# Kernel tuning notes

Measured on AMD Instinct MI355X. Metric: run time of the kernel, lower is better.

Reference implementation:

```python
import jax, jax.numpy as jnp
import numpy as np

V, D, H, L, MAXS = 32000, 768, 12, 6, 2048
HD = D // H  # 64
FF = 4 * D
B, S = 8, 1024
EPS = 1e-5


def _make_pe():
    pos = np.arange(MAXS, dtype=np.float32)[:, None]
    div = np.exp(np.arange(0, D, 2, dtype=np.float32) * (-np.log(10000.0) / D))
    pe = np.zeros((MAXS, D), dtype=np.float32)
    pe[:, 0::2] = np.sin(pos * div)
    pe[:, 1::2] = np.cos(pos * div)
    return jnp.asarray(pe)


def setup_inputs() -> dict:
    key = jax.random.key(0)
    ks = jax.random.split(key, 16)
    sc = 0.02
    return {
        "tokens": jax.random.randint(ks[0], (B, S), 0, V),
        "k_mask": jnp.ones((B, S), dtype=jnp.int32),
        "emb": jax.random.normal(ks[1], (V, D), jnp.float32) * sc,
        "pe": _make_pe(),
        "ln1_s": jnp.ones((L, D), jnp.float32),
        "ln1_b": jnp.zeros((L, D), jnp.float32),
        "wq": jax.random.normal(ks[2], (L, H, D, HD), jnp.float32) * sc,
        "wk": jax.random.normal(ks[3], (L, H, D, HD), jnp.float32) * sc,
        "wv": jax.random.normal(ks[4], (L, H, D, HD), jnp.float32) * sc,
        "wo": jax.random.normal(ks[5], (L, D, D), jnp.float32) * sc,
        "ln2_s": jnp.ones((L, D), jnp.float32),
        "ln2_b": jnp.zeros((L, D), jnp.float32),
        "w1": jax.random.normal(ks[6], (L, D, FF), jnp.float32) * sc,
        "b1": jnp.zeros((L, FF), jnp.float32),
        "w2": jax.random.normal(ks[7], (L, FF, D), jnp.float32) * sc,
        "b2": jnp.zeros((L, D), jnp.float32),
    }


def _ln(x, s, b):
    m = jnp.mean(x, axis=-1, keepdims=True)
    v = jnp.var(x, axis=-1, keepdims=True)
    return (x - m) * jax.lax.rsqrt(v + EPS) * s + b


def _forward(tokens, k_mask, emb, pe, ln1_s, ln1_b, wq, wk, wv, wo,
             ln2_s, ln2_b, w1, b1, w2, b2):
    x = emb[tokens] + pe[None, :tokens.shape[1], :]  # [B,S,D]
    mask = (k_mask != 0)[:, None, None, :]  # [B,1,1,S]
    for l in range(L):
        xn = _ln(x, ln1_s[l], ln1_b[l])
        q = jnp.einsum('bsd,hde->bhse', xn, wq[l])
        k = jnp.einsum('bsd,hde->bhse', xn, wk[l])
        v = jnp.einsum('bsd,hde->bhse', xn, wv[l])
        scores = jnp.einsum('bhse,bhte->bhst', q, k) / (HD ** 0.5)
        scores = jnp.where(mask, scores, -jnp.inf)
        attn = jax.nn.softmax(scores, axis=-1)
        o = jnp.einsum('bhst,bhte->bhse', attn, v)  # [B,H,S,HD]
        o = o.transpose(0, 2, 1, 3).reshape(x.shape)  # concat heads -> [B,S,D]
        x = x + o @ wo[l]
        xn = _ln(x, ln2_s[l], ln2_b[l])
        h = jax.nn.gelu(xn @ w1[l] + b1[l], approximate=False)
        x = x + h @ w2[l] + b2[l]
    return x


def reference(tokens, k_mask, emb, pe, ln1_s, ln1_b, wq, wk, wv, wo,
              ln2_s, ln2_b, w1, b1, w2, b2):
    return _forward(tokens, k_mask, emb, pe, ln1_s, ln1_b, wq, wk, wv, wo,
                    ln2_s, ln2_b, w1, b1, w2, b2)
```

## Files before the change

kernel.cpp:

```cpp
#include <hip/hip_runtime.h>
#include <math.h>

typedef unsigned short u16;
typedef unsigned int u32;
typedef __attribute__((ext_vector_type(8))) __bf16 bf16x8;
typedef __attribute__((ext_vector_type(4))) float f32x4;
typedef __attribute__((ext_vector_type(8))) unsigned short ushort8v;
typedef __attribute__((ext_vector_type(4))) float float4v;
typedef __attribute__((ext_vector_type(4))) unsigned short u16x4;

typedef const __attribute__((address_space(1))) void gvoid_t;
typedef __attribute__((address_space(3))) void lvoid_t;

#define MFMA(a, b, c) __builtin_amdgcn_mfma_f32_16x16x32_bf16((a), (b), (c), 0, 0, 0)

__device__ __forceinline__ u16 f2bf(float f) {
  __bf16 h = (__bf16)f;
  return __builtin_bit_cast(u16, h);
}

__device__ __forceinline__ void stage64(const u16* g, int ldg, u16* lds, int rows, int tid) {
  int w = tid >> 6, l = tid & 63;
  int lr = l >> 3;
  int cb = (l & 7) << 4;
  for (int it = 0; it < rows; it += 32) {
    int rbase = it + w * 8;
    int r = rbase + lr;
    int scb = cb ^ ((r & 7) << 4);
    const char* gp = (const char*)(g + (size_t)r * ldg) + scb;
    char* lp = (char*)lds + (size_t)rbase * 128;
    __builtin_amdgcn_global_load_lds((gvoid_t*)gp, (lvoid_t*)lp, 16, 0, 0);
  }
}

__device__ __forceinline__ bf16x8 ldsfrag(const u16* base, int row, int e0) {
  int boff = row * 128 + (((e0) << 1) ^ ((row & 7) << 4));
  return *(const bf16x8*)((const char*)base + boff);
}

__global__ void embed_kernel(const int* __restrict__ tok, const float* __restrict__ emb,
                             const float* __restrict__ pe, float* __restrict__ xf) {
  int row = blockIdx.x;
  int tid = threadIdx.x;
  int t = tok[row];
  int spos = row & 1023;
  float4v e = ((const float4v*)(emb + (size_t)t * 768))[tid];
  float4v p = ((const float4v*)(pe + (size_t)spos * 768))[tid];
  float4v r;
  r.x = e.x + p.x; r.y = e.y + p.y; r.z = e.z + p.z; r.w = e.w + p.w;
  ((float4v*)(xf + (size_t)row * 768))[tid] = r;
}

__global__ void ln_kernel(const float* __restrict__ x, const float* __restrict__ sc,
                          const float* __restrict__ bi, u16* __restrict__ out) {
  int row = blockIdx.x;
  int tid = threadIdx.x;
  float4v v = ((const float4v*)(x + (size_t)row * 768))[tid];
  float s = v.x + v.y + v.z + v.w;
  float s2 = v.x * v.x + v.y * v.y + v.z * v.z + v.w * v.w;
  #pragma unroll
  for (int off = 32; off >= 1; off >>= 1) {
    s += __shfl_down(s, off);
    s2 += __shfl_down(s2, off);
  }
  __shared__ float red[8];
  if ((tid & 63) == 0) { red[tid >> 6] = s; red[4 + (tid >> 6)] = s2; }
  __syncthreads();
  float S = red[0] + red[1] + red[2];
  float S2 = red[4] + red[5] + red[6];
  float m = S * (1.0f / 768.0f);
  float var = S2 * (1.0f / 768.0f) - m * m;
  float rs = rsqrtf(var + 1e-5f);
  float4v sv = ((const float4v*)sc)[tid];
  float4v bv = ((const float4v*)bi)[tid];
  u16x4 ov;
  ov.x = f2bf((v.x - m) * rs * sv.x + bv.x);
  ov.y = f2bf((v.y - m) * rs * sv.y + bv.y);
  ov.z = f2bf((v.z - m) * rs * sv.z + bv.z);
  ov.w = f2bf((v.w - m) * rs * sv.w + bv.w);
  *(u16x4*)(out + (size_t)row * 768 + tid * 4) = ov;
}

__global__ void convT_kernel(const float* __restrict__ src, u16* __restrict__ dst,
                             int N, int K, long long sz, long long dz) {
  src += (size_t)blockIdx.z * sz;
  dst += (size_t)blockIdx.z * dz;
  __shared__ float t[32][33];
  int n0 = blockIdx.x * 32, k0 = blockIdx.y * 32;
  int tid = threadIdx.x;
  int tx = tid & 31, ty = tid >> 5;
  for (int r = ty; r < 32; r += 8) t[r][tx] = src[(size_t)(k0 + r) * N + n0 + tx];
  __syncthreads();
  for (int r = ty; r < 32; r += 8) dst[(size_t)(n0 + r) * K + k0 + tx] = f2bf(t[tx][r]);
}

__global__ void convqkvT_kernel(const float* __restrict__ wq, const float* __restrict__ wk,
                                const float* __restrict__ wv, u16* __restrict__ dst,
                                long long wz, long long dz) {
  __shared__ float t[32][33];
  int n0 = blockIdx.x * 32, k0 = blockIdx.y * 32;
  int which = n0 / 768;
  int r0 = n0 % 768;
  int h = r0 >> 6, e0 = r0 & 63;
  const float* src = which == 0 ? wq : (which == 1 ? wk : wv);
  src += (size_t)blockIdx.z * wz;
  dst += (size_t)blockIdx.z * dz;
  int tid = threadIdx.x;
  int tx = tid & 31, ty = tid >> 5;
  for (int r = ty; r < 32; r += 8) t[r][tx] = src[(size_t)(h * 768 + k0 + r) * 64 + e0 + tx];
  __syncthreads();
  for (int r = ty; r < 32; r += 8) dst[(size_t)(n0 + r) * 768 + k0 + tx] = f2bf(t[tx][r]);
}

__global__ void transpose_v_kernel(const u16* __restrict__ v, u16* __restrict__ vt) {
  __shared__ u16 t[64][72];
  int bh = blockIdx.x, sc = blockIdx.y;
  int tid = threadIdx.x;
  const u16* src = v + ((size_t)bh * 1024 + sc * 64) * 64;
  int sl = tid >> 2, e0 = (tid & 3) * 16;
  ushort8v a = *(const ushort8v*)(src + (size_t)sl * 64 + e0);
  ushort8v b = *(const ushort8v*)(src + (size_t)sl * 64 + e0 + 8);
  #pragma unroll
  for (int j = 0; j < 8; ++j) t[sl][e0 + j] = a[j];
  #pragma unroll
  for (int j = 0; j < 8; ++j) t[sl][e0 + 8 + j] = b[j];
  __syncthreads();
  int e = tid >> 2, s0 = (tid & 3) * 16;
  ushort8v o0, o1;
  #pragma unroll
  for (int j = 0; j < 8; ++j) o0[j] = t[s0 + j][e];
  #pragma unroll
  for (int j = 0; j < 8; ++j) o1[j] = t[s0 + 8 + j][e];
  u16* dst = vt + ((size_t)bh * 64 + e) * 1024 + sc * 64 + s0;
  *(ushort8v*)dst = o0;
  *(ushort8v*)(dst + 8) = o1;
}

template <int MODE, int NK>
__global__ __launch_bounds__(256) void gemm128(
    const u16* __restrict__ A, int lda, const u16* __restrict__ Wt, int ldb, int kOuter,
    float* __restrict__ xf, u16* __restrict__ outb, const float* __restrict__ bias,
    u16* __restrict__ qb, u16* __restrict__ kb, u16* __restrict__ vb) {
  __shared__ alignas(16) u16 As[128 * 64];
  __shared__ alignas(16) u16 Bs[128 * 64];
  int tid = threadIdx.x, lane = tid & 63, w = tid >> 6;
  int wm = w >> 1, wn = w & 1;
  int m0 = blockIdx.x * 128, n0 = blockIdx.y * 128;
  f32x4 acc[4][4] = {};
  int lr = lane >> 3;
  int cb = (lane & 7) << 4;
  int sws = cb ^ (lr << 4);
  const char* pA = (const char*)(A + (size_t)m0 * lda) + (size_t)(w * 8 + lr) * (lda * 2) + sws;
  const char* pB = (const char*)(Wt + (size_t)n0 * ldb) + (size_t)(w * 8 + lr) * (ldb * 2) + sws;
  char* dA = (char*)As + w * 1024;
  char* dB = (char*)Bs + w * 1024;
  int arow = wm * 64 + (lane & 15);
  int brow = wn * 64 + (lane & 15);
  int e0 = (lane >> 4) * 8;
  for (int c = 0; c < kOuter; ++c) {
    #pragma unroll
    for (int kt = 0; kt < NK; ++kt) {
      __syncthreads();
      #pragma unroll
      for (int i = 0; i < 4; ++i) {
        __builtin_amdgcn_global_load_lds((gvoid_t*)(pA + (size_t)i * 32 * (lda * 2)),
                                         (lvoid_t*)(dA + i * 4096), 16, 0, 0);
        __builtin_amdgcn_global_load_lds((gvoid_t*)(pB + (size_t)i * 32 * (ldb * 2)),
                                         (lvoid_t*)(dB + i * 4096), 16, 0, 0);
      }
      pA += 128; pB += 128;
      __syncthreads();
      #pragma unroll
      for (int kk = 0; kk < 2; ++kk) {
        bf16x8 af[4], bfr[4];
        #pragma unroll
        for (int mt = 0; mt < 4; ++mt) af[mt] = ldsfrag(As, arow + mt * 16, kk * 32 + e0);
        #pragma unroll
        for (int nt = 0; nt < 4; ++nt) bfr[nt] = ldsfrag(Bs, brow + nt * 16, kk * 32 + e0);
        #pragma unroll
        for (int mt = 0; mt < 4; ++mt)
          #pragma unroll
          for (int nt = 0; nt < 4; ++nt)
            acc[mt][nt] = MFMA(af[mt], bfr[nt], acc[mt][nt]);
      }
    }
  }
  int rbase = m0 + wm * 64 + ((lane >> 4) << 2);
  int cbase = n0 + wn * 64 + (lane & 15);
  if constexpr (MODE == 0) {
    int which = n0 / 768;
    u16* dstb = which == 0 ? qb : (which == 1 ? kb : vb);
    int cloc = cbase - which * 768;
    #pragma unroll
    for (int mt = 0; mt < 4; ++mt) {
      #pragma unroll
      for (int nt = 0; nt < 4; ++nt) {
        int rr = cloc + nt * 16;
        int h = rr >> 6, e = rr & 63;
        #pragma unroll
        for (int reg = 0; reg < 4; ++reg) {
          int row = rbase + mt * 16 + reg;
          int b = row >> 10, s = row & 1023;
          dstb[((size_t)(b * 12 + h) * 1024 + s) * 64 + e] = f2bf(acc[mt][nt][reg]);
        }
      }
    }
  } else if constexpr (MODE == 2) {
    #pragma unroll
    for (int mt = 0; mt < 4; ++mt) {
      #pragma unroll
      for (int nt = 0; nt < 4; ++nt) {
        int col = cbase + nt * 16;
        float bb = bias[col];
        #pragma unroll
        for (int reg = 0; reg < 4; ++reg) {
          int row = rbase + mt * 16 + reg;
          float t = acc[mt][nt][reg] + bb;
          float u = t * fmaf(t * t, 0.044715f, 1.0f);
          float ex = __builtin_amdgcn_exp2f(u * -2.3022156f);
          float g = t * __builtin_amdgcn_rcpf(1.0f + ex);
          outb[(size_t)row * 3072 + col] = f2bf(g);
        }
      }
    }
  } else {
    #pragma unroll
    for (int mt = 0; mt < 4; ++mt) {
      #pragma unroll
      for (int nt = 0; nt < 4; ++nt) {
        int col = cbase + nt * 16;
        float bb = (MODE == 3) ? bias[col] : 0.0f;
        #pragma unroll
        for (int reg = 0; reg < 4; ++reg) {
          int row = rbase + mt * 16 + reg;
          xf[(size_t)row * 768 + col] += acc[mt][nt][reg] + bb;
        }
      }
    }
  }
}

__global__ __launch_bounds__(256) void flash64(
    const u16* __restrict__ q, const u16* __restrict__ k, const u16* __restrict__ vt,
    const int* __restrict__ kmask, u16* __restrict__ o) {
  __shared__ alignas(16) u16 Qs[64 * 64];
  __shared__ alignas(16) u16 Ks[2][64 * 64];
  __shared__ alignas(16) u16 Vs[2][64 * 64];
  __shared__ alignas(16) u16 Ps[64 * 64];
  int tid = threadIdx.x, lane = tid & 63, w = tid >> 6;
  int lc = lane & 15;
  int bh = blockIdx.x, q0 = blockIdx.y * 64;
  int b = bh / 12, h = bh % 12;

  stage64(q + ((size_t)bh * 1024 + q0) * 64, 64, Qs, 64, tid);
  __syncthreads();
  int qrow = w * 16 + lc;
  int e0 = (lane >> 4) * 8;
  bf16x8 aq0 = ldsfrag(Qs, qrow, e0);
  bf16x8 aq1 = ldsfrag(Qs, qrow, 32 + e0);

  bf16x8 ones;
  #pragma unroll
  for (int j = 0; j < 8; ++j) ones[j] = (__bf16)1.0f;

  f32x4 oacc[4] = {};
  f32x4 lacc = {};
  const float SCL = 0.125f * 1.44269504f;
  const float SH = -3.0f * 1.44269504f;
  int prow_base = w * 16 + ((lane >> 4) << 2);

  stage64(k + (size_t)bh * 1024 * 64, 64, Ks[0], 64, tid);
  stage64(vt + (size_t)bh * 64 * 1024, 1024, Vs[0], 64, tid);

  for (int kt = 0; kt < 16; ++kt) {
    asm volatile("s_waitcnt vmcnt(0)" ::: "memory");
    __builtin_amdgcn_sched_barrier(0);
    __builtin_amdgcn_s_barrier();
    __builtin_amdgcn_sched_barrier(0);
    const u16* Kc = Ks[kt & 1];
    const u16* Vc = Vs[kt & 1];

    f32x4 sacc[4] = {};
    #pragma unroll
    for (int nt = 0; nt < 4; ++nt) {
      bf16x8 bk = ldsfrag(Kc, nt * 16 + lc, e0);
      sacc[nt] = MFMA(aq0, bk, sacc[nt]);
    }
    #pragma unroll
    for (int nt = 0; nt < 4; ++nt) {
      bf16x8 bk = ldsfrag(Kc, nt * 16 + lc, 32 + e0);
      sacc[nt] = MFMA(aq1, bk, sacc[nt]);
    }

    if (kt + 1 < 16) {
      stage64(k + ((size_t)bh * 1024 + (kt + 1) * 64) * 64, 64, Ks[(kt + 1) & 1], 64, tid);
      stage64(vt + (size_t)bh * 64 * 1024 + (kt + 1) * 64, 1024, Vs[(kt + 1) & 1], 64, tid);
    }

    #pragma unroll
    for (int nt = 0; nt < 4; ++nt) {
      int c = nt * 16 + lc;
      float mk = kmask[b * 1024 + kt * 64 + c] ? SH : -1e30f;
      #pragma unroll
      for (int r = 0; r < 4; ++r) {
        float p = __builtin_amdgcn_exp2f(fmaf(sacc[nt][r], SCL, mk));
        int prow = prow_base + r;
        int boff = prow * 128 + ((c << 1) ^ ((prow & 7) << 4));
        *(u16*)((char*)Ps + boff) = f2bf(p);
      }
    }

    bf16x8 ap0 = ldsfrag(Ps, qrow, e0);
    bf16x8 ap1 = ldsfrag(Ps, qrow, 32 + e0);
    lacc = MFMA(ap0, ones, lacc);
    lacc = MFMA(ap1, ones, lacc);
    #pragma unroll
    for (int et = 0; et < 4; ++et) {
      bf16x8 bv = ldsfrag(Vc, et * 16 + lc, e0);
      oacc[et] = MFMA(ap0, bv, oacc[et]);
    }
    #pragma unroll
    for (int et = 0; et < 4; ++et) {
      bf16x8 bv = ldsfrag(Vc, et * 16 + lc, 32 + e0);
      oacc[et] = MFMA(ap1, bv, oacc[et]);
    }
  }

  float rl[4];
  #pragma unroll
  for (int r = 0; r < 4; ++r) rl[r] = __builtin_amdgcn_rcpf(lacc[r]);
  int orow_base = q0 + prow_base;
  #pragma unroll
  for (int et = 0; et < 4; ++et) {
    int e = et * 16 + lc;
    #pragma unroll
    for (int r = 0; r < 4; ++r) {
      int row = orow_base + r;
      o[((size_t)(b * 1024 + row)) * 768 + h * 64 + e] = f2bf(oacc[et][r] * rl[r]);
    }
  }
}

__global__ void copy_kernel(const float* __restrict__ src, float* __restrict__ dst) {
  size_t i = (size_t)blockIdx.x * blockDim.x + threadIdx.x;
  ((float4v*)dst)[i] = ((const float4v*)src)[i];
}

extern "C" void kernel_launch(void* const* d_in, const int* in_sizes, int n_in,
                              void* d_out, int out_size, void* d_ws, size_t ws_size,
                              hipStream_t stream) {
  const int* tokens = (const int*)d_in[0];
  const int* kmask = (const int*)d_in[1];
  const float* emb = (const float*)d_in[2];
  const float* pe = (const float*)d_in[3];
  const float* ln1_s = (const float*)d_in[4];
  const float* ln1_b = (const float*)d_in[5];
  const float* wq = (const float*)d_in[6];
  const float* wk = (const float*)d_in[7];
  const float* wv = (const float*)d_in[8];
  const float* wo = (const float*)d_in[9];
  const float* ln2_s = (const float*)d_in[10];
  const float* ln2_b = (const float*)d_in[11];
  const float* w1 = (const float*)d_in[12];
  const float* b1 = (const float*)d_in[13];
  const float* w2 = (const float*)d_in[14];
  const float* b2 = (const float*)d_in[15];

  char* ws = (char*)d_ws;
  float* xf = (float*)ws;
  u16* xn   = (u16*)(ws + 25165824);
  u16* qb   = (u16*)(ws + 37748736);
  u16* kb   = (u16*)(ws + 50331648);
  u16* vb   = (u16*)(ws + 62914560);
  u16* vtb  = (u16*)(ws + 75497472);
  u16* ob   = (u16*)(ws + 88080384);
  u16* ffh  = (u16*)(ws + 100663296);

  const size_t SZ_QKV = (size_t)2304 * 768;
  const size_t SZ_O   = (size_t)768 * 768;
  const size_t SZ_F1  = (size_t)3072 * 768;
  const size_t SZ_F2  = (size_t)768 * 3072;
  const size_t NEED = 150994944 + 2 * 6 * (SZ_QKV + SZ_O + SZ_F1 + SZ_F2);
  bool pre = ws_size >= NEED;
  int nz = pre ? 6 : 1;
  u16* wqkvt = (u16*)(ws + 150994944);
  u16* wot   = wqkvt + (size_t)nz * SZ_QKV;
  u16* w1t   = wot + (size_t)nz * SZ_O;
  u16* w2t   = w1t + (size_t)nz * SZ_F1;

  embed_kernel<<<8192, 192, 0, stream>>>(tokens, emb, pe, xf);

  if (pre) {
    convqkvT_kernel<<<dim3(72, 24, 6), 256, 0, stream>>>(wq, wk, wv, wqkvt, 589824LL, (long long)SZ_QKV);
    convT_kernel<<<dim3(24, 24, 6), 256, 0, stream>>>(wo, wot, 768, 768, 589824LL, (long long)SZ_O);
    convT_kernel<<<dim3(96, 24, 6), 256, 0, stream>>>(w1, w1t, 3072, 768, 2359296LL, (long long)SZ_F1);
    convT_kernel<<<dim3(24, 96, 6), 256, 0, stream>>>(w2, w2t, 768, 3072, 2359296LL, (long long)SZ_F2);
  }

  for (int l = 0; l < 6; ++l) {
    size_t woff_qkv = (size_t)l * 12 * 768 * 64;
    size_t woff_o = (size_t)l * 768 * 768;
    size_t woff_ff = (size_t)l * 768 * 3072;
    const u16* wt_qkv_l = wqkvt + (pre ? (size_t)l * SZ_QKV : 0);
    const u16* wt_o_l   = wot   + (pre ? (size_t)l * SZ_O   : 0);
    const u16* wt_1_l   = w1t   + (pre ? (size_t)l * SZ_F1  : 0);
    const u16* wt_2_l   = w2t   + (pre ? (size_t)l * SZ_F2  : 0);

    if (!pre) {
      convqkvT_kernel<<<dim3(72, 24, 1), 256, 0, stream>>>(wq + woff_qkv, wk + woff_qkv, wv + woff_qkv, (u16*)wt_qkv_l, 0LL, 0LL);
      convT_kernel<<<dim3(24, 24, 1), 256, 0, stream>>>(wo + woff_o, (u16*)wt_o_l, 768, 768, 0LL, 0LL);
      convT_kernel<<<dim3(96, 24, 1), 256, 0, stream>>>(w1 + woff_ff, (u16*)wt_1_l, 3072, 768, 0LL, 0LL);
      convT_kernel<<<dim3(24, 96, 1), 256, 0, stream>>>(w2 + woff_ff, (u16*)wt_2_l, 768, 3072, 0LL, 0LL);
    }

    ln_kernel<<<8192, 192, 0, stream>>>(xf, ln1_s + l * 768, ln1_b + l * 768, xn);
    gemm128<0, 6><<<dim3(64, 18, 1), 256, 0, stream>>>(xn, 768, wt_qkv_l, 768, 2, nullptr, nullptr, nullptr, qb, kb, vb);
    transpose_v_kernel<<<dim3(96, 16), 256, 0, stream>>>(vb, vtb);
    flash64<<<dim3(96, 16), 256, 0, stream>>>(qb, kb, vtb, kmask, ob);
    gemm128<1, 6><<<dim3(64, 6, 1), 256, 0, stream>>>(ob, 768, wt_o_l, 768, 2, xf, nullptr, nullptr, nullptr, nullptr, nullptr);
    ln_kernel<<<8192, 192, 0, stream>>>(xf, ln2_s + l * 768, ln2_b + l * 768, xn);
    gemm128<2, 6><<<dim3(64, 24, 1), 256, 0, stream>>>(xn, 768, wt_1_l, 768, 2, nullptr, ffh, b1 + l * 3072, nullptr, nullptr, nullptr);
    gemm128<3, 6><<<dim3(64, 6, 1), 256, 0, stream>>>(ffh, 3072, wt_2_l, 3072, 8, xf, nullptr, b2 + l * 768, nullptr, nullptr, nullptr);
  }

  copy_kernel<<<6144, 256, 0, stream>>>(xf, (float*)d_out);
}
```

Baseline: 1.594 ms.

## Use 128-query flash tiles, 64-wide N tiles for D-output GEMMs, fuse final copy

Flash attention now processes 128 query rows per block (two 64-row halves per wave), so each staged K/V tile is reused twice and the K/V loads per query are halved. The Q tile is staged through the Ps and Ks buffers to save LDS. The output-projection and FFN2 GEMMs use 64-wide N tiles, doubling their block count (384 to 768) to fill more CUs. The final copy kernel is removed by having the last FFN2 epilogue also write its result to the output buffer. The trade-offs are fewer attention blocks (768), more register pressure from the doubled accumulators, and lower per-block MFMA density in the narrow GEMMs.

```diff
diff --git a/kernel.cpp b/kernel.cpp
--- a/kernel.cpp
+++ b/kernel.cpp
@@ -136,17 +136,20 @@
   *(ushort8v*)(dst + 8) = o1;
 }
 
-template <int MODE, int NK>
+template <int MODE, int NK, int BN>
 __global__ __launch_bounds__(256) void gemm128(
     const u16* __restrict__ A, int lda, const u16* __restrict__ Wt, int ldb, int kOuter,
     float* __restrict__ xf, u16* __restrict__ outb, const float* __restrict__ bias,
-    u16* __restrict__ qb, u16* __restrict__ kb, u16* __restrict__ vb) {
+    u16* __restrict__ qb, u16* __restrict__ kb, u16* __restrict__ vb,
+    float* __restrict__ outf) {
+  constexpr int NT = BN / 32;
+  constexpr int NBAND = BN / 2;
   __shared__ alignas(16) u16 As[128 * 64];
-  __shared__ alignas(16) u16 Bs[128 * 64];
+  __shared__ alignas(16) u16 Bs[BN * 64];
   int tid = threadIdx.x, lane = tid & 63, w = tid >> 6;
   int wm = w >> 1, wn = w & 1;
-  int m0 = blockIdx.x * 128, n0 = blockIdx.y * 128;
-  f32x4 acc[4][4] = {};
+  int m0 = blockIdx.x * 128, n0 = blockIdx.y * BN;
+  f32x4 acc[4][NT] = {};
   int lr = lane >> 3;
   int cb = (lane & 7) << 4;
   int sws = cb ^ (lr << 4);
@@ -155,38 +158,39 @@
   char* dA = (char*)As + w * 1024;
   char* dB = (char*)Bs + w * 1024;
   int arow = wm * 64 + (lane & 15);
-  int brow = wn * 64 + (lane & 15);
+  int brow = wn * NBAND + (lane & 15);
   int e0 = (lane >> 4) * 8;
   for (int c = 0; c < kOuter; ++c) {
     #pragma unroll
     for (int kt = 0; kt < NK; ++kt) {
       __syncthreads();
       #pragma unroll
-      for (int i = 0; i < 4; ++i) {
+      for (int i = 0; i < 4; ++i)
         __builtin_amdgcn_global_load_lds((gvoid_t*)(pA + (size_t)i * 32 * (lda * 2)),
                                          (lvoid_t*)(dA + i * 4096), 16, 0, 0);
+      #pragma unroll
+      for (int i = 0; i < BN / 32; ++i)
         __builtin_amdgcn_global_load_lds((gvoid_t*)(pB + (size_t)i * 32 * (ldb * 2)),
                                          (lvoid_t*)(dB + i * 4096), 16, 0, 0);
-      }
       pA += 128; pB += 128;
       __syncthreads();
       #pragma unroll
       for (int kk = 0; kk < 2; ++kk) {
-        bf16x8 af[4], bfr[4];
+        bf16x8 af[4], bfr[NT];
         #pragma unroll
         for (int mt = 0; mt < 4; ++mt) af[mt] = ldsfrag(As, arow + mt * 16, kk * 32 + e0);
         #pragma unroll
-        for (int nt = 0; nt < 4; ++nt) bfr[nt] = ldsfrag(Bs, brow + nt * 16, kk * 32 + e0);
+        for (int nt = 0; nt < NT; ++nt) bfr[nt] = ldsfrag(Bs, brow + nt * 16, kk * 32 + e0);
         #pragma unroll
         for (int mt = 0; mt < 4; ++mt)
           #pragma unroll
-          for (int nt = 0; nt < 4; ++nt)
+          for (int nt = 0; nt < NT; ++nt)
             acc[mt][nt] = MFMA(af[mt], bfr[nt], acc[mt][nt]);
       }
     }
   }
   int rbase = m0 + wm * 64 + ((lane >> 4) << 2);
-  int cbase = n0 + wn * 64 + (lane & 15);
+  int cbase = n0 + wn * NBAND + (lane & 15);
   if constexpr (MODE == 0) {
     int which = n0 / 768;
     u16* dstb = which == 0 ? qb : (which == 1 ? kb : vb);
@@ -194,7 +198,7 @@
     #pragma unroll
     for (int mt = 0; mt < 4; ++mt) {
       #pragma unroll
-      for (int nt = 0; nt < 4; ++nt) {
+      for (int nt = 0; nt < NT; ++nt) {
         int rr = cloc + nt * 16;
         int h = rr >> 6, e = rr & 63;
         #pragma unroll
@@ -209,7 +213,7 @@
     #pragma unroll
     for (int mt = 0; mt < 4; ++mt) {
       #pragma unroll
-      for (int nt = 0; nt < 4; ++nt) {
+      for (int nt = 0; nt < NT; ++nt) {
         int col = cbase + nt * 16;
         float bb = bias[col];
         #pragma unroll
@@ -227,44 +231,51 @@
     #pragma unroll
     for (int mt = 0; mt < 4; ++mt) {
       #pragma unroll
-      for (int nt = 0; nt < 4; ++nt) {
+      for (int nt = 0; nt < NT; ++nt) {
         int col = cbase + nt * 16;
         float bb = (MODE == 3) ? bias[col] : 0.0f;
         #pragma unroll
         for (int reg = 0; reg < 4; ++reg) {
           int row = rbase + mt * 16 + reg;
-          xf[(size_t)row * 768 + col] += acc[mt][nt][reg] + bb;
+          size_t idx = (size_t)row * 768 + col;
+          float nv = xf[idx] + acc[mt][nt][reg] + bb;
+          xf[idx] = nv;
+          if (MODE == 3 && outf) outf[idx] = nv;
         }
       }
     }
   }
 }
 
-__global__ __launch_bounds__(256) void flash64(
+__global__ __launch_bounds__(256) void flash128(
     const u16* __restrict__ q, const u16* __restrict__ k, const u16* __restrict__ vt,
     const int* __restrict__ kmask, u16* __restrict__ o) {
-  __shared__ alignas(16) u16 Qs[64 * 64];
   __shared__ alignas(16) u16 Ks[2][64 * 64];
   __shared__ alignas(16) u16 Vs[2][64 * 64];
   __shared__ alignas(16) u16 Ps[64 * 64];
   int tid = threadIdx.x, lane = tid & 63, w = tid >> 6;
   int lc = lane & 15;
-  int bh = blockIdx.x, q0 = blockIdx.y * 64;
-  int b = bh / 12, h = bh % 12;
-
-  stage64(q + ((size_t)bh * 1024 + q0) * 64, 64, Qs, 64, tid);
+  int bh = blockIdx.x, q0 = blockIdx.y * 128;
+  int b = bh / 12, hd = bh % 12;
+
+  stage64(q + ((size_t)bh * 1024 + q0) * 64, 64, Ps, 64, tid);
+  stage64(q + ((size_t)bh * 1024 + q0 + 64) * 64, 64, Ks[0], 64, tid);
   __syncthreads();
   int qrow = w * 16 + lc;
   int e0 = (lane >> 4) * 8;
-  bf16x8 aq0 = ldsfrag(Qs, qrow, e0);
-  bf16x8 aq1 = ldsfrag(Qs, qrow, 32 + e0);
+  bf16x8 aq[2][2];
+  aq[0][0] = ldsfrag(Ps, qrow, e0);
+  aq[0][1] = ldsfrag(Ps, qrow, 32 + e0);
+  aq[1][0] = ldsfrag(Ks[0], qrow, e0);
+  aq[1][1] = ldsfrag(Ks[0], qrow, 32 + e0);
+  __syncthreads();
 
   bf16x8 ones;
   #pragma unroll
   for (int j = 0; j < 8; ++j) ones[j] = (__bf16)1.0f;
 
-  f32x4 oacc[4] = {};
-  f32x4 lacc = {};
+  f32x4 oacc[2][4] = {};
+  f32x4 lacc[2] = {};
   const float SCL = 0.125f * 1.44269504f;
   const float SH = -3.0f * 1.44269504f;
   int prow_base = w * 16 + ((lane >> 4) << 2);
@@ -280,16 +291,15 @@
     const u16* Kc = Ks[kt & 1];
     const u16* Vc = Vs[kt & 1];
 
-    f32x4 sacc[4] = {};
+    f32x4 sacc[2][4] = {};
     #pragma unroll
     for (int nt = 0; nt < 4; ++nt) {
-      bf16x8 bk = ldsfrag(Kc, nt * 16 + lc, e0);
-      sacc[nt] = MFMA(aq0, bk, sacc[nt]);
-    }
-    #pragma unroll
-    for (int nt = 0; nt < 4; ++nt) {
-      bf16x8 bk = ldsfrag(Kc, nt * 16 + lc, 32 + e0);
-      sacc[nt] = MFMA(aq1, bk, sacc[nt]);
+      bf16x8 bk0 = ldsfrag(Kc, nt * 16 + lc, e0);
+      bf16x8 bk1 = ldsfrag(Kc, nt * 16 + lc, 32 + e0);
+      sacc[0][nt] = MFMA(aq[0][0], bk0, sacc[0][nt]);
+      sacc[0][nt] = MFMA(aq[0][1], bk1, sacc[0][nt]);
+      sacc[1][nt] = MFMA(aq[1][0], bk0, sacc[1][nt]);
+      sacc[1][nt] = MFMA(aq[1][1], bk1, sacc[1][nt]);
     }
 
     if (kt + 1 < 16) {
@@ -297,53 +307,57 @@
       stage64(vt + (size_t)bh * 64 * 1024 + (kt + 1) * 64, 1024, Vs[(kt + 1) & 1], 64, tid);
     }
 
-    #pragma unroll
-    for (int nt = 0; nt < 4; ++nt) {
-      int c = nt * 16 + lc;
-      float mk = kmask[b * 1024 + kt * 64 + c] ? SH : -1e30f;
+    float mkv[4];
+    #pragma unroll
+    for (int nt = 0; nt < 4; ++nt)
+      mkv[nt] = kmask[b * 1024 + kt * 64 + nt * 16 + lc] ? SH : -1e30f;
+
+    #pragma unroll
+    for (int h = 0; h < 2; ++h) {
+      #pragma unroll
+      for (int nt = 0; nt < 4; ++nt) {
+        int c = nt * 16 + lc;
+        #pragma unroll
+        for (int r = 0; r < 4; ++r) {
+          float p = __builtin_amdgcn_exp2f(fmaf(sacc[h][nt][r], SCL, mkv[nt]));
+          int prow = prow_base + r;
+          int boff = prow * 128 + ((c << 1) ^ ((prow & 7) << 4));
+          *(u16*)((char*)Ps + boff) = f2bf(p);
+        }
+      }
+      bf16x8 ap0 = ldsfrag(Ps, qrow, e0);
+      bf16x8 ap1 = ldsfrag(Ps, qrow, 32 + e0);
+      lacc[h] = MFMA(ap0, ones, lacc[h]);
+      lacc[h] = MFMA(ap1, ones, lacc[h]);
+      #pragma unroll
+      for (int et = 0; et < 4; ++et) {
+        bf16x8 bv = ldsfrag(Vc, et * 16 + lc, e0);
+        oacc[h][et] = MFMA(ap0, bv, oacc[h][et]);
+      }
+      #pragma unroll
+      for (int et = 0; et < 4; ++et) {
+        bf16x8 bv = ldsfrag(Vc, et * 16 + lc, 32 + e0);
+        oacc[h][et] = MFMA(ap1, bv, oacc[h][et]);
+      }
+    }
+  }
+
+  #pragma unroll
+  for (int h = 0; h < 2; ++h) {
+    float rl[4];
+    #pragma unroll
+    for (int r = 0; r < 4; ++r) rl[r] = __builtin_amdgcn_rcpf(lacc[h][r]);
+    int orow_base = q0 + h * 64 + prow_base;
+    #pragma unroll
+    for (int et = 0; et < 4; ++et) {
+      int e = et * 16 + lc;
       #pragma unroll
       for (int r = 0; r < 4; ++r) {
-        float p = __builtin_amdgcn_exp2f(fmaf(sacc[nt][r], SCL, mk));
-        int prow = prow_base + r;
-        int boff = prow * 128 + ((c << 1) ^ ((prow & 7) << 4));
-        *(u16*)((char*)Ps + boff) = f2bf(p);
-      }
-    }
-
-    bf16x8 ap0 = ldsfrag(Ps, qrow, e0);
-    bf16x8 ap1 = ldsfrag(Ps, qrow, 32 + e0);
-    lacc = MFMA(ap0, ones, lacc);
-    lacc = MFMA(ap1, ones, lacc);
-    #pragma unroll
-    for (int et = 0; et < 4; ++et) {
-      bf16x8 bv = ldsfrag(Vc, et * 16 + lc, e0);
-      oacc[et] = MFMA(ap0, bv, oacc[et]);
-    }
-    #pragma unroll
-    for (int et = 0; et < 4; ++et) {
-      bf16x8 bv = ldsfrag(Vc, et * 16 + lc, 32 + e0);
-      oacc[et] = MFMA(ap1, bv, oacc[et]);
-    }
-  }
-
-  float rl[4];
-  #pragma unroll
-  for (int r = 0; r < 4; ++r) rl[r] = __builtin_amdgcn_rcpf(lacc[r]);
-  int orow_base = q0 + prow_base;
-  #pragma unroll
-  for (int et = 0; et < 4; ++et) {
-    int e = et * 16 + lc;
-    #pragma unroll
-    for (int r = 0; r < 4; ++r) {
-      int row = orow_base + r;
-      o[((size_t)(b * 1024 + row)) * 768 + h * 64 + e] = f2bf(oacc[et][r] * rl[r]);
-    }
-  }
-}
-
-__global__ void copy_kernel(const float* __restrict__ src, float* __restrict__ dst) {
-  size_t i = (size_t)blockIdx.x * blockDim.x + threadIdx.x;
-  ((float4v*)dst)[i] = ((const float4v*)src)[i];
+        int row = orow_base + r;
+        o[((size_t)(b * 1024 + row)) * 768 + hd * 64 + e] = f2bf(oacc[h][et][r] * rl[r]);
+      }
+    }
+  }
 }
 
 extern "C" void kernel_launch(void* const* d_in, const int* in_sizes, int n_in,
@@ -414,14 +428,13 @@
     }
 
     ln_kernel<<<8192, 192, 0, stream>>>(xf, ln1_s + l * 768, ln1_b + l * 768, xn);
-    gemm128<0, 6><<<dim3(64, 18, 1), 256, 0, stream>>>(xn, 768, wt_qkv_l, 768, 2, nullptr, nullptr, nullptr, qb, kb, vb);
+    gemm128<0, 6, 128><<<dim3(64, 18, 1), 256, 0, stream>>>(xn, 768, wt_qkv_l, 768, 2, nullptr, nullptr, nullptr, qb, kb, vb, nullptr);
     transpose_v_kernel<<<dim3(96, 16), 256, 0, stream>>>(vb, vtb);
-    flash64<<<dim3(96, 16), 256, 0, stream>>>(qb, kb, vtb, kmask, ob);
-    gemm128<1, 6><<<dim3(64, 6, 1), 256, 0, stream>>>(ob, 768, wt_o_l, 768, 2, xf, nullptr, nullptr, nullptr, nullptr, nullptr);
+    flash128<<<dim3(96, 8), 256, 0, stream>>>(qb, kb, vtb, kmask, ob);
+    gemm128<1, 6, 64><<<dim3(64, 12, 1), 256, 0, stream>>>(ob, 768, wt_o_l, 768, 2, xf, nullptr, nullptr, nullptr, nullptr, nullptr, nullptr);
     ln_kernel<<<8192, 192, 0, stream>>>(xf, ln2_s + l * 768, ln2_b + l * 768, xn);
-    gemm128<2, 6><<<dim3(64, 24, 1), 256, 0, stream>>>(xn, 768, wt_1_l, 768, 2, nullptr, ffh, b1 + l * 3072, nullptr, nullptr, nullptr);
-    gemm128<3, 6><<<dim3(64, 6, 1), 256, 0, stream>>>(ffh, 3072, wt_2_l, 3072, 8, xf, nullptr, b2 + l * 768, nullptr, nullptr, nullptr);
-  }
-
-  copy_kernel<<<6144, 256, 0, stream>>>(xf, (float*)d_out);
-}
+    gemm128<2, 6, 128><<<dim3(64, 24, 1), 256, 0, stream>>>(xn, 768, wt_1_l, 768, 2, nullptr, ffh, b1 + l * 3072, nullptr, nullptr, nullptr, nullptr);
+    gemm128<3, 6, 64><<<dim3(64, 12, 1), 256, 0, stream>>>(ffh, 3072, wt_2_l, 3072, 8, xf, nullptr, b2 + l * 768, nullptr, nullptr, nullptr,
+                                                           (l == 5) ? (float*)d_out : nullptr);
+  }
+}
```

Measured after the change: 1.541 ms. 1.03x faster.
